# Optimization experiments

Measured on AMD Instinct MI355X. Metric: run time of the kernel, lower is better.

Reference implementation:

```python
import jax, jax.numpy as jnp
import numpy as np

NUM_VAR = 8
NUM_SET = [3, 3, 3, 3, 3, 3, 3, 3]
TOTAL = int(np.prod(NUM_SET))          # 6561 rules
SUM_SET = int(np.sum(NUM_SET))          # 24 membership functions
BATCH = 2048

# var index for each membership-function row k
VAR_IDX = np.repeat(np.arange(NUM_VAR), NUM_SET)  # (SUM_SET,)
# mem_out row used by rule r for variable i: offset_i + r // (TOTAL // num_set[i])
_offsets = np.concatenate([[0], np.cumsum(NUM_SET)[:-1]])
_r = np.arange(TOTAL)
MEM_INDEX = np.stack([_offsets[i] + _r // (TOTAL // NUM_SET[i]) for i in range(NUM_VAR)])  # (NUM_VAR, TOTAL)
J_LAST = NUM_SET[-1] - 1  # stale-j bug in original concat loop


def setup_inputs() -> dict:
    key = jax.random.key(0)
    k1, k2, k3 = jax.random.split(key, 3)
    return {
        "input": jax.random.normal(k1, (NUM_VAR, BATCH), dtype=jnp.float32),
        "premise_params": jax.random.uniform(k2, (SUM_SET, 3), dtype=jnp.float32),
        "conseq_params": jax.random.normal(k3, (TOTAL * (NUM_VAR + 1), 1), dtype=jnp.float32),
    }


def reference(input, premise_params, conseq_params):
    B = input.shape[1]
    a = premise_params[:, 0:1]  # (SUM_SET,1)
    b = premise_params[:, 1:2]
    c = premise_params[:, 2:3]
    # generalized bell membership, all (SUM_SET, B) at once
    x = ((input[VAR_IDX] - c) / a) ** 2
    mem_out = 1.0 / (1.0 + x ** b)
    # segmented product fire strength: prod over variables of gathered memberships
    fire_strength = jnp.prod(mem_out[MEM_INDEX], axis=0)  # (TOTAL, B)
    fire_strength = fire_strength / jnp.sum(fire_strength)  # scalar-sum normalization (as in original)
    input_with_bias = jnp.concatenate([input, jnp.ones((1, B), input.dtype)], axis=0)  # (NUM_VAR+1, B)
    # faithful to original bug: block 0 uses fs[0], blocks 1..TOTAL-1 all use fs[J_LAST]
    w = jnp.concatenate(
        [fire_strength[0:1], jnp.broadcast_to(fire_strength[J_LAST], (TOTAL - 1, B))], axis=0
    )  # (TOTAL, B)
    fsi = (w[:, None, :] * input_with_bias[None, :, :]).reshape(TOTAL * (NUM_VAR + 1), B)
    A = fsi.T  # (B, TOTAL*(NUM_VAR+1))
    return A @ conseq_params  # (B, 1)
```

## Files before the change

### kernel.cpp

```cpp
#include <hip/hip_runtime.h>
#include <math.h>


#define NVAR 8
#define TOTALJ 6561
#define NB 2048
#define K1_BLOCKS 64
#define K1_THREADS 256
#define K2_BLOCKS 8
#define K2_THREADS 256

#define WS_SV    0
#define WS_SSUM  576
#define WS_F0    640

__global__ __launch_bounds__(K1_THREADS) void anfis_k1(
    const float* __restrict__ input,
    const float* __restrict__ premise,
    const float* __restrict__ conseq,
    float* __restrict__ ws)
{
    const int t    = threadIdx.x;
    const int g    = blockIdx.x;
    const int gt   = g * K1_THREADS + t;
    const int wave = t >> 6;
    const int lane = t & 63;

    float sv[9];
    #pragma unroll
    for (int v = 0; v < 9; ++v) sv[v] = 0.0f;
    if (gt < TOTALJ) {
        const float* row = conseq + gt * 9;
        #pragma unroll
        for (int v = 0; v < 9; ++v) sv[v] = row[v];
    }
    #pragma unroll
    for (int v = 0; v < 9; ++v) {
        #pragma unroll
        for (int m = 32; m; m >>= 1) sv[v] += __shfl_xor(sv[v], m);
    }
    __shared__ float s_sv[4][9];
    if (lane == 0) {
        #pragma unroll
        for (int v = 0; v < 9; ++v) s_sv[wave][v] = sv[v];
    }

    const int i  = t & 7;
    const int bl = t >> 3;
    const int b  = g * 32 + bl;

    const float x = input[i * NB + b];
    float m3[3];
    #pragma unroll
    for (int d = 0; d < 3; ++d) {
        const int k = 3 * i + d;
        const float pa = premise[k * 3 + 0];
        const float pb = premise[k * 3 + 1];
        const float pc = premise[k * 3 + 2];
        const float tt = (x - pc) / pa;
        const float x2 = tt * tt;
        m3[d] = 1.0f / (1.0f + powf(x2, pb));
    }
    #pragma unroll
    for (int d = 0; d < 3; ++d) {
        m3[d] *= __shfl_xor(m3[d], 1);
        m3[d] *= __shfl_xor(m3[d], 2);
        m3[d] *= __shfl_xor(m3[d], 4);
    }
    if (i == 0) ws[WS_F0 + b] = m3[0];

    float contrib = (i == 0) ? (m3[0] + m3[1] + m3[2]) : 0.0f;
    #pragma unroll
    for (int m = 32; m; m >>= 1) contrib += __shfl_xor(contrib, m);
    __shared__ float s_c[4];
    if (lane == 0) s_c[wave] = contrib;

    __syncthreads();
    if (t < 9) {
        ws[WS_SV + g * 9 + t] = s_sv[0][t] + s_sv[1][t] + s_sv[2][t] + s_sv[3][t];
    }
    if (t == 9) {
        ws[WS_SSUM + g] = s_c[0] + s_c[1] + s_c[2] + s_c[3];
    }
}

__global__ __launch_bounds__(K2_THREADS) void anfis_k2(
    const float* __restrict__ input,
    const float* __restrict__ ws,
    float* __restrict__ out)
{
    __shared__ float s_Sv[9];
    __shared__ float s_invS;
    const int t = threadIdx.x;

    if (t < 9) {
        float s = 0.0f;
        #pragma unroll 8
        for (int g = 0; g < K1_BLOCKS; ++g) s += ws[WS_SV + g * 9 + t];
        s_Sv[t] = s;
    }
    if (t >= 64 && t < 128) {
        float s = ws[WS_SSUM + (t - 64)];
        #pragma unroll
        for (int m = 32; m; m >>= 1) s += __shfl_xor(s, m);
        if (t == 64) s_invS = 1.0f / (2187.0f * s);
    }
    __syncthreads();

    const int b = blockIdx.x * K2_THREADS + t;
    float D = s_Sv[8];
    #pragma unroll
    for (int v = 0; v < 8; ++v) D += input[v * NB + b] * s_Sv[v];
    out[b] = ws[WS_F0 + b] * D * s_invS;
}

extern "C" void kernel_launch(void* const* d_in, const int* in_sizes, int n_in,
                              void* d_out, int out_size, void* d_ws, size_t ws_size,
                              hipStream_t stream) {
    const float* input   = (const float*)d_in[0];
    const float* premise = (const float*)d_in[1];
    const float* conseq  = (const float*)d_in[2];
    float* out = (float*)d_out;
    float* ws  = (float*)d_ws;

    anfis_k1<<<K1_BLOCKS, K1_THREADS, 0, stream>>>(input, premise, conseq, ws);
    anfis_k2<<<K2_BLOCKS, K2_THREADS, 0, stream>>>(input, ws, out);
}
```

Baseline: 62.94 us.

## Fuse two kernels into one redundant-per-block kernel with fast intrinsics

Replaces the two-kernel pipeline with a single launch of 8 blocks of 1024 threads. Each block redundantly recomputes the full conseq column sums (read as float4) and all membership products for the whole batch in shared memory, then writes its own 256 outputs. This removes the second launch and the global workspace round trip. Membership math switches to hardware rcp/exp2/log2 intrinsics in place of division and powf. The cost is 8x redundant work per block and low occupancy, plus lower-precision transcendentals.

```diff
diff --git a/kernel.cpp b/kernel.cpp
--- a/kernel.cpp
+++ b/kernel.cpp
@@ -2,116 +2,111 @@
 #include <math.h>
 
 
-#define NVAR 8
-#define TOTALJ 6561
 #define NB 2048
-#define K1_BLOCKS 64
-#define K1_THREADS 256
-#define K2_BLOCKS 8
-#define K2_THREADS 256
 
-#define WS_SV    0
-#define WS_SSUM  576
-#define WS_F0    640
+__device__ __forceinline__ float fast_rcp(float x) { return __builtin_amdgcn_rcpf(x); }
+__device__ __forceinline__ float fast_exp2(float x) { return __builtin_amdgcn_exp2f(x); }
+__device__ __forceinline__ float fast_log2(float x) { return __builtin_amdgcn_logf(x); }
 
-__global__ __launch_bounds__(K1_THREADS) void anfis_k1(
+__global__ __launch_bounds__(1024) void anfis_fused(
     const float* __restrict__ input,
     const float* __restrict__ premise,
     const float* __restrict__ conseq,
-    float* __restrict__ ws)
+    float* __restrict__ out)
 {
     const int t    = threadIdx.x;
-    const int g    = blockIdx.x;
-    const int gt   = g * K1_THREADS + t;
+    const int lane = t & 63;
     const int wave = t >> 6;
-    const int lane = t & 63;
+
+    __shared__ float s_F0[NB];
+    __shared__ float s_svp[16][9];
+    __shared__ float s_sp[16];
+    __shared__ float s_Sv[9];
+    __shared__ float s_invS;
 
     float sv[9];
     #pragma unroll
     for (int v = 0; v < 9; ++v) sv[v] = 0.0f;
-    if (gt < TOTALJ) {
-        const float* row = conseq + gt * 9;
+    const float4* c4 = (const float4*)conseq;
+    for (int g = t; g < 1640; g += 1024) {
+        const float4* base = c4 + g * 9;
         #pragma unroll
-        for (int v = 0; v < 9; ++v) sv[v] = row[v];
+        for (int q = 0; q < 9; ++q) {
+            float4 f = base[q];
+            sv[(4*q + 0) % 9] += f.x;
+            sv[(4*q + 1) % 9] += f.y;
+            sv[(4*q + 2) % 9] += f.z;
+            sv[(4*q + 3) % 9] += f.w;
+        }
     }
+    if (t == 0) {
+        #pragma unroll
+        for (int v = 0; v < 9; ++v) sv[v] += conseq[59040 + v];
+    }
+
+    float inva[24], pb2[24], pc[24];
     #pragma unroll
-    for (int v = 0; v < 9; ++v) {
+    for (int k = 0; k < 24; ++k) {
+        inva[k] = fast_rcp(premise[3*k + 0]);
+        pb2[k]  = 2.0f * premise[3*k + 1];
+        pc[k]   = premise[3*k + 2];
+    }
+
+    float Ssum = 0.0f;
+    #pragma unroll
+    for (int pass = 0; pass < 2; ++pass) {
+        const int b = t + pass * 1024;
+        float P0 = 1.0f, P1 = 1.0f, P2 = 1.0f;
         #pragma unroll
-        for (int m = 32; m; m >>= 1) sv[v] += __shfl_xor(sv[v], m);
+        for (int i = 0; i < 8; ++i) {
+            const float x = input[i * NB + b];
+            #pragma unroll
+            for (int d = 0; d < 3; ++d) {
+                const int k = 3*i + d;
+                const float tt = (x - pc[k]) * inva[k];
+                const float y = fast_exp2(pb2[k] * fast_log2(__builtin_fabsf(tt)));
+                const float e = 1.0f + y;
+                if (d == 0) P0 *= e; else if (d == 1) P1 *= e; else P2 *= e;
+            }
+        }
+        const float F0 = fast_rcp(P0);
+        s_F0[b] = F0;
+        Ssum += F0 + fast_rcp(P1) + fast_rcp(P2);
     }
-    __shared__ float s_sv[4][9];
+
+    #pragma unroll
+    for (int m = 32; m; m >>= 1) {
+        #pragma unroll
+        for (int v = 0; v < 9; ++v) sv[v] += __shfl_xor(sv[v], m);
+        Ssum += __shfl_xor(Ssum, m);
+    }
     if (lane == 0) {
         #pragma unroll
-        for (int v = 0; v < 9; ++v) s_sv[wave][v] = sv[v];
+        for (int v = 0; v < 9; ++v) s_svp[wave][v] = sv[v];
+        s_sp[wave] = Ssum;
     }
-
-    const int i  = t & 7;
-    const int bl = t >> 3;
-    const int b  = g * 32 + bl;
-
-    const float x = input[i * NB + b];
-    float m3[3];
-    #pragma unroll
-    for (int d = 0; d < 3; ++d) {
-        const int k = 3 * i + d;
-        const float pa = premise[k * 3 + 0];
-        const float pb = premise[k * 3 + 1];
-        const float pc = premise[k * 3 + 2];
-        const float tt = (x - pc) / pa;
-        const float x2 = tt * tt;
-        m3[d] = 1.0f / (1.0f + powf(x2, pb));
-    }
-    #pragma unroll
-    for (int d = 0; d < 3; ++d) {
-        m3[d] *= __shfl_xor(m3[d], 1);
-        m3[d] *= __shfl_xor(m3[d], 2);
-        m3[d] *= __shfl_xor(m3[d], 4);
-    }
-    if (i == 0) ws[WS_F0 + b] = m3[0];
-
-    float contrib = (i == 0) ? (m3[0] + m3[1] + m3[2]) : 0.0f;
-    #pragma unroll
-    for (int m = 32; m; m >>= 1) contrib += __shfl_xor(contrib, m);
-    __shared__ float s_c[4];
-    if (lane == 0) s_c[wave] = contrib;
-
     __syncthreads();
     if (t < 9) {
-        ws[WS_SV + g * 9 + t] = s_sv[0][t] + s_sv[1][t] + s_sv[2][t] + s_sv[3][t];
-    }
-    if (t == 9) {
-        ws[WS_SSUM + g] = s_c[0] + s_c[1] + s_c[2] + s_c[3];
-    }
-}
-
-__global__ __launch_bounds__(K2_THREADS) void anfis_k2(
-    const float* __restrict__ input,
-    const float* __restrict__ ws,
-    float* __restrict__ out)
-{
-    __shared__ float s_Sv[9];
-    __shared__ float s_invS;
-    const int t = threadIdx.x;
-
-    if (t < 9) {
         float s = 0.0f;
-        #pragma unroll 8
-        for (int g = 0; g < K1_BLOCKS; ++g) s += ws[WS_SV + g * 9 + t];
+        #pragma unroll
+        for (int w2 = 0; w2 < 16; ++w2) s += s_svp[w2][t];
         s_Sv[t] = s;
     }
-    if (t >= 64 && t < 128) {
-        float s = ws[WS_SSUM + (t - 64)];
+    if (t == 16) {
+        float s = 0.0f;
         #pragma unroll
-        for (int m = 32; m; m >>= 1) s += __shfl_xor(s, m);
-        if (t == 64) s_invS = 1.0f / (2187.0f * s);
+        for (int w2 = 0; w2 < 16; ++w2) s += s_sp[w2];
+        s_invS = 1.0f / (2187.0f * s);
     }
     __syncthreads();
 
-    const int b = blockIdx.x * K2_THREADS + t;
-    float D = s_Sv[8];
-    #pragma unroll
-    for (int v = 0; v < 8; ++v) D += input[v * NB + b] * s_Sv[v];
-    out[b] = ws[WS_F0 + b] * D * s_invS;
+    if (t < 256) {
+        const int b = blockIdx.x * 256 + t;
+        float D = s_Sv[8];
+        #pragma unroll
+        for (int v = 0; v < 8; ++v) D += input[v * NB + b] * s_Sv[v];
+        out[b] = s_F0[b] * D * s_invS;
+    }
 }
 
 extern "C" void kernel_launch(void* const* d_in, const int* in_sizes, int n_in,
@@ -121,8 +116,7 @@
     const float* premise = (const float*)d_in[1];
     const float* conseq  = (const float*)d_in[2];
     float* out = (float*)d_out;
-    float* ws  = (float*)d_ws;
+    (void)d_ws; (void)ws_size;
 
-    anfis_k1<<<K1_BLOCKS, K1_THREADS, 0, stream>>>(input, premise, conseq, ws);
-    anfis_k2<<<K2_BLOCKS, K2_THREADS, 0, stream>>>(input, ws, out);
+    anfis_fused<<<8, 1024, 0, stream>>>(input, premise, conseq, out);
 }
```

New measurement: 65.22 us. 1.04x slower.
